# Optimization experiments

Measured on AMD Instinct MI355X. Metric: run time of the kernel, lower is better.

The kernel has to match this reference:

```python
import jax, jax.numpy as jnp
import numpy as np
from jax import lax

N, CIN, COUT = 4, 3, 16
D = H = W = 64
K, S, PAD, OUT_PAD = 3, 2, 1, 1


def setup_inputs() -> dict:
    key = jax.random.key(0)
    k1, k2, k3, k4 = jax.random.split(key, 4)
    x = jax.random.normal(k1, (N, CIN, D, H, W), dtype=jnp.float32)
    # torch ConvTranspose3d weight layout: [Cin, Cout, kD, kH, kW]
    w = jax.random.normal(k2, (CIN, COUT, K, K, K), dtype=jnp.float32) * 0.1
    b = jax.random.normal(k3, (COUT,), dtype=jnp.float32) * 0.1
    subtract = jax.random.normal(k4, (COUT,), dtype=jnp.float32) * 0.1
    return {"x": x, "w": w, "b": b, "subtract": subtract}


def reference(x, w, b, subtract):
    # ConvTranspose3d(k=3, s=2, p=1, output_padding=1) as a dilated conv:
    # flip kernel spatially, swap in/out channel axes, lhs_dilation = stride,
    # padding low = k-1-p = 1, padding high = k-1-p+output_padding = 2.
    w_conv = jnp.flip(jnp.transpose(w, (1, 0, 2, 3, 4)), axis=(2, 3, 4))  # [Cout,Cin,k,k,k]
    y = lax.conv_general_dilated(
        x, w_conv,
        window_strides=(1, 1, 1),
        padding=[(1, 2), (1, 2), (1, 2)],
        lhs_dilation=(S, S, S),
        dimension_numbers=("NCDHW", "OIDHW", "NCDHW"),
    )  # [N, 16, 2D, 2H, 2W]
    y = y + b[None, :, None, None, None]
    # MaxPool3d(kernel=2, stride=2, pad=0)
    y = lax.reduce_window(
        y, -jnp.inf, lax.max,
        window_dimensions=(1, 1, 2, 2, 2),
        window_strides=(1, 1, 2, 2, 2),
        padding="VALID",
    )  # [N, 16, D, H, W]
    s = jax.nn.softmax(y, axis=1)                       # channel softmax
    z = s - subtract[None, :, None, None, None]          # per-channel subtract
    sw = z * jax.nn.sigmoid(z)                           # swish
    return jnp.max(sw, axis=1)                           # max over channels -> [N, D, H, W]
```

## Files before the change

### kernel.cpp

```cpp
#include <hip/hip_runtime.h>
#include <math.h>

#define CIN   3
#define COUT  16
#define DHW   64

__global__ __launch_bounds__(256, 2) void fused_convt_pool_softmax_swish_max(
    const float* __restrict__ x,
    const float* __restrict__ w,
    const float* __restrict__ bias,
    const float* __restrict__ sub,
    float* __restrict__ out)
{
    const int tp = threadIdx.x;
    const int h  = blockIdx.x * blockDim.y + threadIdx.y;
    const int d0 = blockIdx.y * 2;
    const int n  = blockIdx.z;
    const int w0 = tp * 2;

    float xr[CIN][3][2][3];
    const size_t nbase = (size_t)n * CIN * DHW * DHW * DHW;
    const bool w2ok = (w0 + 2 < DHW);
    const int  off2 = w2ok ? 2 : 0;
#pragma unroll
    for (int c = 0; c < CIN; ++c) {
#pragma unroll
        for (int dd = 0; dd < 3; ++dd) {
#pragma unroll
            for (int hh = 0; hh < 2; ++hh) {
                const int id = d0 + dd;
                const int ih = h + hh;
                float v0 = 0.0f, v1 = 0.0f, v2 = 0.0f;
                if (id < DHW && ih < DHW) {
                    const float* row = x + nbase + (((size_t)c * DHW + id) * DHW + ih) * DHW + w0;
                    const float2 a = *(const float2*)row;
                    v0 = a.x;
                    v1 = a.y;
                    const float t = row[off2];
                    v2 = w2ok ? t : 0.0f;
                }
                xr[c][dd][hh][0] = v0;
                xr[c][dd][hh][1] = v1;
                xr[c][dd][hh][2] = v2;
            }
        }
    }

    float pooled[2][2][COUT];
#pragma unroll
    for (int co = 0; co < COUT; ++co) {
        float acc[2][2][2][2][2];
#pragma unroll
        for (int i = 0; i < 32; ++i) (&acc[0][0][0][0][0])[i] = 0.0f;
#pragma unroll
        for (int c = 0; c < CIN; ++c) {
            const float* wg = w + ((size_t)c * COUT + co) * 27;
#pragma unroll
            for (int kd = 0; kd < 3; ++kd) {
                const int pd  = (kd == 1) ? 0 : 1;
                const int dlt = (kd == 0) ? 1 : 0;
#pragma unroll
                for (int kh = 0; kh < 3; ++kh) {
                    const int ph = (kh == 1) ? 0 : 1;
                    const int hh = (kh == 0) ? 1 : 0;
#pragma unroll
                    for (int kw = 0; kw < 3; ++kw) {
                        const int pw = (kw == 1) ? 0 : 1;
                        const int ww = (kw == 0) ? 1 : 0;
                        const float wt = wg[kd * 9 + kh * 3 + kw];
#pragma unroll
                        for (int dout = 0; dout < 2; ++dout) {
                            acc[dout][0][pd][ph][pw] =
                                fmaf(wt, xr[c][dout + dlt][hh][ww],     acc[dout][0][pd][ph][pw]);
                            acc[dout][1][pd][ph][pw] =
                                fmaf(wt, xr[c][dout + dlt][hh][ww + 1], acc[dout][1][pd][ph][pw]);
                        }
                    }
                }
            }
        }
        const float bco = bias[co];
#pragma unroll
        for (int dout = 0; dout < 2; ++dout) {
#pragma unroll
            for (int vx = 0; vx < 2; ++vx) {
                const float* a = &acc[dout][vx][0][0][0];
                const float m01 = fmaxf(a[0], a[1]);
                const float m23 = fmaxf(a[2], a[3]);
                const float m45 = fmaxf(a[4], a[5]);
                const float m67 = fmaxf(a[6], a[7]);
                pooled[dout][vx][co] = fmaxf(fmaxf(m01, m23), fmaxf(m45, m67)) + bco;
            }
        }
    }

#pragma unroll
    for (int dout = 0; dout < 2; ++dout) {
        float res[2];
#pragma unroll
        for (int vx = 0; vx < 2; ++vx) {
            float m = pooled[dout][vx][0];
#pragma unroll
            for (int co = 1; co < COUT; ++co) m = fmaxf(m, pooled[dout][vx][co]);
            float e[COUT];
            float s = 0.0f;
#pragma unroll
            for (int co = 0; co < COUT; ++co) {
                const float ev = __expf(pooled[dout][vx][co] - m);
                e[co] = ev;
                s += ev;
            }
            const float inv = __builtin_amdgcn_rcpf(s);
            float zmax = -3.402823466e+38f;
#pragma unroll
            for (int co = 0; co < COUT; ++co)
                zmax = fmaxf(zmax, fmaf(e[co], inv, -sub[co]));
            res[vx] = zmax * __builtin_amdgcn_rcpf(1.0f + __expf(-zmax));
        }
        float2 r2; r2.x = res[0]; r2.y = res[1];
        float* op = out + (((size_t)n * DHW + (d0 + dout)) * DHW + h) * DHW + w0;
        *(float2*)op = r2;
    }
}

extern "C" void kernel_launch(void* const* d_in, const int* in_sizes, int n_in,
                              void* d_out, int out_size, void* d_ws, size_t ws_size,
                              hipStream_t stream) {
    const float* x   = (const float*)d_in[0];
    const float* w   = (const float*)d_in[1];
    const float* b   = (const float*)d_in[2];
    const float* sub = (const float*)d_in[3];
    float* out = (float*)d_out;

    dim3 block(32, 8, 1);
    dim3 grid(DHW / 8, DHW / 2, 4);
    fused_convt_pool_softmax_swish_max<<<grid, block, 0, stream>>>(x, w, b, sub, out);
}
```

Before: 113.4 us.

## Map lanes to output channels with DPP cross-lane softmax and sliding-window W loop

The kernel now assigns each of 16 lanes in a group to one output channel, not having every thread loop over all 16 channels. Each lane keeps its channel's 81 weights in registers and walks 16 W positions with a rotating three-buffer register window, prefetching the next input column one step ahead. The channel softmax sum and the final channel max become DPP row-rotate reductions across the 16 lanes. The input boundaries are handled by zeroing weights and clamping indices. The exp is now taken without subtracting the channel max first, which risks overflow for large activations, and adds redundant broadcast loads plus per-step cross-lane reductions.

```diff
diff --git a/kernel.cpp b/kernel.cpp
--- a/kernel.cpp
+++ b/kernel.cpp
@@ -1,9 +1,30 @@
 #include <hip/hip_runtime.h>
 #include <math.h>
 
-#define CIN   3
-#define COUT  16
-#define DHW   64
+#define CIN 3
+#define COUT 16
+#define DHW 64
+
+
+template <int CTRL>
+static __device__ __forceinline__ float dpp_rorf(float v) {
+    return __int_as_float(__builtin_amdgcn_update_dpp(
+        0, __float_as_int(v), CTRL, 0xF, 0xF, false));
+}
+static __device__ __forceinline__ float rmax16(float v) {
+    v = fmaxf(v, dpp_rorf<0x128>(v));
+    v = fmaxf(v, dpp_rorf<0x124>(v));
+    v = fmaxf(v, dpp_rorf<0x122>(v));
+    v = fmaxf(v, dpp_rorf<0x121>(v));
+    return v;
+}
+static __device__ __forceinline__ float rsum16(float v) {
+    v = v + dpp_rorf<0x128>(v);
+    v = v + dpp_rorf<0x124>(v);
+    v = v + dpp_rorf<0x122>(v);
+    v = v + dpp_rorf<0x121>(v);
+    return v;
+}
 
 __global__ __launch_bounds__(256, 2) void fused_convt_pool_softmax_swish_max(
     const float* __restrict__ x,
@@ -12,115 +33,131 @@
     const float* __restrict__ sub,
     float* __restrict__ out)
 {
-    const int tp = threadIdx.x;
-    const int h  = blockIdx.x * blockDim.y + threadIdx.y;
-    const int d0 = blockIdx.y * 2;
-    const int n  = blockIdx.z;
-    const int w0 = tp * 2;
+    const int lane = threadIdx.x & 63;
+    const int wv   = threadIdx.x >> 6;
+    const int co   = lane & 15;
+    const int vg   = lane >> 4;
+    const int h    = blockIdx.x * 4 + wv;
+    const int d    = blockIdx.y;
+    const int n    = blockIdx.z;
+    const int w0   = vg * 16;
 
-    float xr[CIN][3][2][3];
-    const size_t nbase = (size_t)n * CIN * DHW * DHW * DHW;
-    const bool w2ok = (w0 + 2 < DHW);
-    const int  off2 = w2ok ? 2 : 0;
+    float wl[CIN][27];
+    {
+        const float* wp = w + co * 27;
 #pragma unroll
-    for (int c = 0; c < CIN; ++c) {
+        for (int c = 0; c < CIN; ++c)
 #pragma unroll
-        for (int dd = 0; dd < 3; ++dd) {
+            for (int k = 0; k < 27; ++k)
+                wl[c][k] = wp[(size_t)c * COUT * 27 + k];
+    }
+    if (d == DHW - 1) {
+#pragma unroll
+        for (int c = 0; c < CIN; ++c)
+#pragma unroll
+            for (int k = 0; k < 9; ++k) wl[c][k] = 0.0f;
+    }
+    if (h == DHW - 1) {
+#pragma unroll
+        for (int c = 0; c < CIN; ++c)
+#pragma unroll
+            for (int kd = 0; kd < 3; ++kd)
+#pragma unroll
+                for (int kw = 0; kw < 3; ++kw) wl[c][kd * 9 + kw] = 0.0f;
+    }
+    const float bco = bias[co];
+    const float sco = sub[co];
+
+    const float* xn = x + (size_t)n * CIN * DHW * DHW * DHW;
+    int voff[12];
+#pragma unroll
+    for (int c = 0; c < CIN; ++c)
+#pragma unroll
+        for (int dd = 0; dd < 2; ++dd)
 #pragma unroll
             for (int hh = 0; hh < 2; ++hh) {
-                const int id = d0 + dd;
-                const int ih = h + hh;
-                float v0 = 0.0f, v1 = 0.0f, v2 = 0.0f;
-                if (id < DHW && ih < DHW) {
-                    const float* row = x + nbase + (((size_t)c * DHW + id) * DHW + ih) * DHW + w0;
-                    const float2 a = *(const float2*)row;
-                    v0 = a.x;
-                    v1 = a.y;
-                    const float t = row[off2];
-                    v2 = w2ok ? t : 0.0f;
+                const int id = min(d + dd, DHW - 1);
+                const int ih = min(h + hh, DHW - 1);
+                voff[(c * 2 + dd) * 2 + hh] = ((c * DHW + id) * DHW + ih) * DHW + w0;
+            }
+
+    float X0[12], X1[12], X2[12];
+#pragma unroll
+    for (int r = 0; r < 12; ++r) X0[r] = xn[voff[r]];
+#pragma unroll
+    for (int r = 0; r < 12; ++r) X1[r] = xn[voff[r] + 1];
+
+    float res = 0.0f;
+
+    auto step = [&](int i, float (&CUR)[12], float (&NXT)[12], float (&LD)[12],
+                    bool do_load, bool last_load) {
+        if (do_load) {
+            if (!last_load) {
+#pragma unroll
+                for (int r = 0; r < 12; ++r) LD[r] = xn[voff[r] + i + 2];
+            } else {
+                const int eo = (vg == 3) ? 15 : 16;
+#pragma unroll
+                for (int r = 0; r < 12; ++r) {
+                    const float t = xn[voff[r] + eo];
+                    LD[r] = (vg == 3) ? 0.0f : t;
                 }
-                xr[c][dd][hh][0] = v0;
-                xr[c][dd][hh][1] = v1;
-                xr[c][dd][hh][2] = v2;
             }
         }
-    }
-
-    float pooled[2][2][COUT];
+        float acc[8];
 #pragma unroll
-    for (int co = 0; co < COUT; ++co) {
-        float acc[2][2][2][2][2];
+        for (int q = 0; q < 8; ++q) acc[q] = 0.0f;
 #pragma unroll
-        for (int i = 0; i < 32; ++i) (&acc[0][0][0][0][0])[i] = 0.0f;
-#pragma unroll
-        for (int c = 0; c < CIN; ++c) {
-            const float* wg = w + ((size_t)c * COUT + co) * 27;
+        for (int c = 0; c < CIN; ++c)
 #pragma unroll
             for (int kd = 0; kd < 3; ++kd) {
-                const int pd  = (kd == 1) ? 0 : 1;
-                const int dlt = (kd == 0) ? 1 : 0;
+                const int dd = (kd == 0) ? 1 : 0;
+                const int pd = (kd == 1) ? 0 : 1;
 #pragma unroll
                 for (int kh = 0; kh < 3; ++kh) {
+                    const int hh = (kh == 0) ? 1 : 0;
                     const int ph = (kh == 1) ? 0 : 1;
-                    const int hh = (kh == 0) ? 1 : 0;
+                    const int r  = (c * 2 + dd) * 2 + hh;
 #pragma unroll
                     for (int kw = 0; kw < 3; ++kw) {
                         const int pw = (kw == 1) ? 0 : 1;
-                        const int ww = (kw == 0) ? 1 : 0;
-                        const float wt = wg[kd * 9 + kh * 3 + kw];
-#pragma unroll
-                        for (int dout = 0; dout < 2; ++dout) {
-                            acc[dout][0][pd][ph][pw] =
-                                fmaf(wt, xr[c][dout + dlt][hh][ww],     acc[dout][0][pd][ph][pw]);
-                            acc[dout][1][pd][ph][pw] =
-                                fmaf(wt, xr[c][dout + dlt][hh][ww + 1], acc[dout][1][pd][ph][pw]);
-                        }
+                        const float xv = (kw == 0) ? NXT[r] : CUR[r];
+                        const int   qi = (pd * 2 + ph) * 2 + pw;
+                        acc[qi] = fmaf(wl[c][kd * 9 + kh * 3 + kw], xv, acc[qi]);
                     }
                 }
             }
-        }
-        const float bco = bias[co];
+        float p = acc[0];
 #pragma unroll
-        for (int dout = 0; dout < 2; ++dout) {
-#pragma unroll
-            for (int vx = 0; vx < 2; ++vx) {
-                const float* a = &acc[dout][vx][0][0][0];
-                const float m01 = fmaxf(a[0], a[1]);
-                const float m23 = fmaxf(a[2], a[3]);
-                const float m45 = fmaxf(a[4], a[5]);
-                const float m67 = fmaxf(a[6], a[7]);
-                pooled[dout][vx][co] = fmaxf(fmaxf(m01, m23), fmaxf(m45, m67)) + bco;
-            }
-        }
-    }
+        for (int q = 1; q < 8; ++q) p = fmaxf(p, acc[q]);
+        p += bco;
+        const float e   = __expf(p);
+        const float s   = rsum16(e);
+        const float inv = __builtin_amdgcn_rcpf(s);
+        const float z   = fmaf(e, inv, -sco);
+        const float zm  = rmax16(z);
+        const float r_  = zm * __builtin_amdgcn_rcpf(1.0f + __expf(-zm));
+        if (co == i) res = r_;
+    };
 
-#pragma unroll
-    for (int dout = 0; dout < 2; ++dout) {
-        float res[2];
-#pragma unroll
-        for (int vx = 0; vx < 2; ++vx) {
-            float m = pooled[dout][vx][0];
-#pragma unroll
-            for (int co = 1; co < COUT; ++co) m = fmaxf(m, pooled[dout][vx][co]);
-            float e[COUT];
-            float s = 0.0f;
-#pragma unroll
-            for (int co = 0; co < COUT; ++co) {
-                const float ev = __expf(pooled[dout][vx][co] - m);
-                e[co] = ev;
-                s += ev;
-            }
-            const float inv = __builtin_amdgcn_rcpf(s);
-            float zmax = -3.402823466e+38f;
-#pragma unroll
-            for (int co = 0; co < COUT; ++co)
-                zmax = fmaxf(zmax, fmaf(e[co], inv, -sub[co]));
-            res[vx] = zmax * __builtin_amdgcn_rcpf(1.0f + __expf(-zmax));
-        }
-        float2 r2; r2.x = res[0]; r2.y = res[1];
-        float* op = out + (((size_t)n * DHW + (d0 + dout)) * DHW + h) * DHW + w0;
-        *(float2*)op = r2;
-    }
+    step( 0, X0, X1, X2, true,  false);
+    step( 1, X1, X2, X0, true,  false);
+    step( 2, X2, X0, X1, true,  false);
+    step( 3, X0, X1, X2, true,  false);
+    step( 4, X1, X2, X0, true,  false);
+    step( 5, X2, X0, X1, true,  false);
+    step( 6, X0, X1, X2, true,  false);
+    step( 7, X1, X2, X0, true,  false);
+    step( 8, X2, X0, X1, true,  false);
+    step( 9, X0, X1, X2, true,  false);
+    step(10, X1, X2, X0, true,  false);
+    step(11, X2, X0, X1, true,  false);
+    step(12, X0, X1, X2, true,  false);
+    step(13, X1, X2, X0, true,  false);
+    step(14, X2, X0, X1, true,  true );
+    step(15, X0, X1, X2, false, false);
+
+    out[(((size_t)n * DHW + d) * DHW + h) * DHW + lane] = res;
 }
 
 extern "C" void kernel_launch(void* const* d_in, const int* in_sizes, int n_in,
@@ -132,7 +169,7 @@
     const float* sub = (const float*)d_in[3];
     float* out = (float*)d_out;
 
-    dim3 block(32, 8, 1);
-    dim3 grid(DHW / 8, DHW / 2, 4);
+    dim3 block(256, 1, 1);
+    dim3 grid(DHW / 4, DHW, 4);
     fused_convt_pool_softmax_swish_max<<<grid, block, 0, stream>>>(x, w, b, sub, out);
 }
```

After: 117.2 us. 3.4% more time.

## Double-buffer weight scalar loads with inline asm software pipeline

Applied to the files above, without the earlier changes.

Replaces compiler-generated weight loads with explicit s_load_dwordx8 scalar loads into two SGPR buffers. A template-recursive pipeline issues the next (cin,cout) group's weights while the current group's FMAs run, using sched_barrier and explicit lgkmcnt waits. It also drops the zero-initialisation by writing the first tap's product directly, and moves the bias add to after pooling. This needs many SGPRs and relies on inline asm being scheduled correctly.

```diff
diff --git a/kernel.cpp b/kernel.cpp
--- a/kernel.cpp
+++ b/kernel.cpp
@@ -1,11 +1,112 @@
 #include <hip/hip_runtime.h>
 #include <math.h>
 
-#define CIN   3
-#define COUT  16
-#define DHW   64
-
-__global__ __launch_bounds__(256, 2) void fused_convt_pool_softmax_swish_max(
+#define CIN 3
+#define COUT 16
+#define DHW 64
+
+
+typedef float f8 __attribute__((ext_vector_type(8)));
+typedef float f2 __attribute__((ext_vector_type(2)));
+
+struct WBuf { f8 a, b, c; f2 d2; float dl; };
+
+template <int G>
+static __device__ __forceinline__ void wload(WBuf& b, const float* wbase) {
+    constexpr int CO = G / 3, C = G % 3;
+    constexpr int BOFF = (C * COUT + CO) * 27 * 4;
+    asm volatile(
+        "s_load_dwordx8 %0, %5, %6\n\t"
+        "s_load_dwordx8 %1, %5, %7\n\t"
+        "s_load_dwordx8 %2, %5, %8\n\t"
+        "s_load_dwordx2 %3, %5, %9\n\t"
+        "s_load_dword   %4, %5, %10"
+        : "=s"(b.a), "=s"(b.b), "=s"(b.c), "=s"(b.d2), "=s"(b.dl)
+        : "s"(wbase), "i"(BOFF), "i"(BOFF + 32), "i"(BOFF + 64),
+          "i"(BOFF + 96), "i"(BOFF + 104));
+}
+
+static __device__ __forceinline__ void wwait(WBuf& b) {
+    asm volatile("s_waitcnt lgkmcnt(0)"
+                 : "+s"(b.a), "+s"(b.b), "+s"(b.c), "+s"(b.d2), "+s"(b.dl));
+}
+
+static __device__ __forceinline__ float welem(const WBuf& w, int k) {
+    return k < 8 ? w.a[k] : k < 16 ? w.b[k - 8] : k < 24 ? w.c[k - 16]
+                 : k < 26 ? w.d2[k - 24] : w.dl;
+}
+
+template <int C>
+static __device__ __forceinline__ void fma_group(
+    const WBuf& wb, const float (&xr)[CIN][3][2][3], float (&acc)[8][4]) {
+#pragma unroll
+    for (int kd = 0; kd < 3; ++kd) {
+        const int pd  = (kd == 1) ? 0 : 1;
+        const int dlt = (kd == 0) ? 1 : 0;
+#pragma unroll
+        for (int kh = 0; kh < 3; ++kh) {
+            const int ph = (kh == 1) ? 0 : 1;
+            const int hh = (kh == 0) ? 1 : 0;
+#pragma unroll
+            for (int kw = 0; kw < 3; ++kw) {
+                const int pw = (kw == 1) ? 0 : 1;
+                const int ww = (kw == 0) ? 1 : 0;
+                const float wt = welem(wb, kd * 9 + kh * 3 + kw);
+                const int q = (pd * 2 + ph) * 2 + pw;
+#pragma unroll
+                for (int dout = 0; dout < 2; ++dout)
+#pragma unroll
+                    for (int vx = 0; vx < 2; ++vx) {
+                        const float xv = xr[C][dout + dlt][hh][ww + vx];
+                        const int v = dout * 2 + vx;
+                        if (C == 0 && kd < 2 && kh < 2 && kw < 2)
+                            acc[q][v] = wt * xv;
+                        else
+                            acc[q][v] = fmaf(wt, xv, acc[q][v]);
+                    }
+            }
+        }
+    }
+}
+
+static __device__ __forceinline__ void pool_close(const float (&acc)[8][4],
+                                                  float (&pc)[4]) {
+#pragma unroll
+    for (int v = 0; v < 4; ++v) {
+        const float m01 = fmaxf(acc[0][v], acc[1][v]);
+        const float m23 = fmaxf(acc[2][v], acc[3][v]);
+        const float m45 = fmaxf(acc[4][v], acc[5][v]);
+        const float m67 = fmaxf(acc[6][v], acc[7][v]);
+        pc[v] = fmaxf(fmaxf(m01, m23), fmaxf(m45, m67));
+    }
+}
+
+template <int G>
+struct Pipe {
+    static __device__ __forceinline__ void run(
+        WBuf& A, WBuf& B, const float* w, const float (&xr)[CIN][3][2][3],
+        float (&acc)[8][4], float (&pooled)[COUT][4]) {
+        constexpr int CO = G / 3, C = G % 3;
+        WBuf& CUR = (G & 1) ? B : A;
+        WBuf& NXT = (G & 1) ? A : B;
+        wwait(CUR);
+        __builtin_amdgcn_sched_barrier(0);
+        if constexpr (G + 1 < CIN * COUT) wload<G + 1>(NXT, w);
+        fma_group<C>(CUR, xr, acc);
+        if constexpr (C == 2) pool_close(acc, pooled[CO]);
+        Pipe<G + 1>::run(A, B, w, xr, acc, pooled);
+    }
+};
+template <>
+struct Pipe<CIN * COUT> {
+    static __device__ __forceinline__ void run(
+        WBuf&, WBuf&, const float*, const float (&)[CIN][3][2][3],
+        float (&)[8][4], float (&)[COUT][4]) {}
+};
+
+__global__ __launch_bounds__(256)
+__attribute__((amdgpu_waves_per_eu(2, 2)))
+void fused_convt_pool_softmax_swish_max(
     const float* __restrict__ x,
     const float* __restrict__ w,
     const float* __restrict__ bias,
@@ -23,16 +124,17 @@
     const bool w2ok = (w0 + 2 < DHW);
     const int  off2 = w2ok ? 2 : 0;
 #pragma unroll
-    for (int c = 0; c < CIN; ++c) {
-#pragma unroll
-        for (int dd = 0; dd < 3; ++dd) {
+    for (int c = 0; c < CIN; ++c)
+#pragma unroll
+        for (int dd = 0; dd < 3; ++dd)
 #pragma unroll
             for (int hh = 0; hh < 2; ++hh) {
                 const int id = d0 + dd;
                 const int ih = h + hh;
                 float v0 = 0.0f, v1 = 0.0f, v2 = 0.0f;
                 if (id < DHW && ih < DHW) {
-                    const float* row = x + nbase + (((size_t)c * DHW + id) * DHW + ih) * DHW + w0;
+                    const float* row =
+                        x + nbase + (((size_t)c * DHW + id) * DHW + ih) * DHW + w0;
                     const float2 a = *(const float2*)row;
                     v0 = a.x;
                     v1 = a.y;
@@ -43,70 +145,30 @@
                 xr[c][dd][hh][1] = v1;
                 xr[c][dd][hh][2] = v2;
             }
-        }
-    }
-
-    float pooled[2][2][COUT];
-#pragma unroll
-    for (int co = 0; co < COUT; ++co) {
-        float acc[2][2][2][2][2];
-#pragma unroll
-        for (int i = 0; i < 32; ++i) (&acc[0][0][0][0][0])[i] = 0.0f;
-#pragma unroll
-        for (int c = 0; c < CIN; ++c) {
-            const float* wg = w + ((size_t)c * COUT + co) * 27;
-#pragma unroll
-            for (int kd = 0; kd < 3; ++kd) {
-                const int pd  = (kd == 1) ? 0 : 1;
-                const int dlt = (kd == 0) ? 1 : 0;
-#pragma unroll
-                for (int kh = 0; kh < 3; ++kh) {
-                    const int ph = (kh == 1) ? 0 : 1;
-                    const int hh = (kh == 0) ? 1 : 0;
-#pragma unroll
-                    for (int kw = 0; kw < 3; ++kw) {
-                        const int pw = (kw == 1) ? 0 : 1;
-                        const int ww = (kw == 0) ? 1 : 0;
-                        const float wt = wg[kd * 9 + kh * 3 + kw];
-#pragma unroll
-                        for (int dout = 0; dout < 2; ++dout) {
-                            acc[dout][0][pd][ph][pw] =
-                                fmaf(wt, xr[c][dout + dlt][hh][ww],     acc[dout][0][pd][ph][pw]);
-                            acc[dout][1][pd][ph][pw] =
-                                fmaf(wt, xr[c][dout + dlt][hh][ww + 1], acc[dout][1][pd][ph][pw]);
-                        }
-                    }
-                }
-            }
-        }
-        const float bco = bias[co];
-#pragma unroll
-        for (int dout = 0; dout < 2; ++dout) {
-#pragma unroll
-            for (int vx = 0; vx < 2; ++vx) {
-                const float* a = &acc[dout][vx][0][0][0];
-                const float m01 = fmaxf(a[0], a[1]);
-                const float m23 = fmaxf(a[2], a[3]);
-                const float m45 = fmaxf(a[4], a[5]);
-                const float m67 = fmaxf(a[6], a[7]);
-                pooled[dout][vx][co] = fmaxf(fmaxf(m01, m23), fmaxf(m45, m67)) + bco;
-            }
-        }
-    }
+
+    float pooled[COUT][4];
+    float acc[8][4];
+    WBuf A, B;
+    wload<0>(A, w);
+    Pipe<0>::run(A, B, w, xr, acc, pooled);
 
 #pragma unroll
     for (int dout = 0; dout < 2; ++dout) {
         float res[2];
 #pragma unroll
         for (int vx = 0; vx < 2; ++vx) {
-            float m = pooled[dout][vx][0];
-#pragma unroll
-            for (int co = 1; co < COUT; ++co) m = fmaxf(m, pooled[dout][vx][co]);
+            const int v = dout * 2 + vx;
+            float pv[COUT];
+#pragma unroll
+            for (int co = 0; co < COUT; ++co) pv[co] = pooled[co][v] + bias[co];
+            float m = pv[0];
+#pragma unroll
+            for (int co = 1; co < COUT; ++co) m = fmaxf(m, pv[co]);
             float e[COUT];
             float s = 0.0f;
 #pragma unroll
             for (int co = 0; co < COUT; ++co) {
-                const float ev = __expf(pooled[dout][vx][co] - m);
+                const float ev = __expf(pv[co] - m);
                 e[co] = ev;
                 s += ev;
             }
```

New measurement: 114.1 us. No clear change (+0.7%).
